# Optimization experiments

Hardware: AMD Instinct MI355X
Metric: run time of the kernel (lower is better)

Reference implementation:

```python
import jax, jax.numpy as jnp
import numpy as np

N0, N1, N2 = 409600, 40960, 4096   # source / mid / target node counts per sampled layer
E1, E2 = 409600, 40960             # edges in layer 1 / layer 2
F_IN, F_HID, F_OUT = 512, 256, 128


def setup_inputs() -> dict:
    key = jax.random.key(0)
    ks = jax.random.split(key, 12)
    s = 1.0 / np.sqrt(F_IN)
    s2 = 1.0 / np.sqrt(F_HID)
    return {
        "x": jax.random.normal(ks[0], (N0, F_IN), dtype=jnp.float32),
        "ei1_src": jax.random.randint(ks[1], (E1,), 0, N0),
        "ei1_dst": jax.random.randint(ks[2], (E1,), 0, N1),
        "ei2_src": jax.random.randint(ks[3], (E2,), 0, N1),
        "ei2_dst": jax.random.randint(ks[4], (E2,), 0, N2),
        "W1l": jax.random.uniform(ks[5], (F_IN, F_HID), jnp.float32, -s, s),
        "b1": jax.random.uniform(ks[6], (F_HID,), jnp.float32, -s, s),
        "W1r": jax.random.uniform(ks[7], (F_IN, F_HID), jnp.float32, -s, s),
        "W2l": jax.random.uniform(ks[8], (F_HID, F_OUT), jnp.float32, -s2, s2),
        "b2": jax.random.uniform(ks[9], (F_OUT,), jnp.float32, -s2, s2),
        "W2r": jax.random.uniform(ks[10], (F_HID, F_OUT), jnp.float32, -s2, s2),
    }


def _sage(x_src, src, dst, n_dst, Wl, b, Wr):
    # PyG SAGEConv (mean aggr): out = lin_l(mean_j x_j) + lin_r(x_target)
    msg = x_src[src]                                           # [E, F] gather
    agg = jax.ops.segment_sum(msg, dst, num_segments=n_dst)    # [n_dst, F]
    cnt = jax.ops.segment_sum(jnp.ones((src.shape[0],), x_src.dtype), dst,
                              num_segments=n_dst)
    mean = agg / jnp.maximum(cnt, 1.0)[:, None]
    x_dst = x_src[:n_dst]                                      # targets are first
    return mean @ Wl + b + x_dst @ Wr


def reference(x, ei1_src, ei1_dst, ei2_src, ei2_dst, W1l, b1, W1r, W2l, b2, W2r):
    h = _sage(x, ei1_src, ei1_dst, N1, W1l, b1, W1r)           # [N1, F_HID]
    h = jax.nn.relu(h)                                         # dropout = identity (eval)
    out = _sage(h, ei2_src, ei2_dst, N2, W2l, b2, W2r)         # [N2, F_OUT]
    return out
```

## Files before the change

kernel.cpp:

```cpp
#include <hip/hip_runtime.h>
#include <hip/hip_bf16.h>

#define N0 409600
#define N1 40960
#define N2 4096
#define E1c 409600
#define E2c 40960
#define F_IN 512
#define F_HID 256
#define F_OUT 128

using bf16x8 = __attribute__((ext_vector_type(8))) short;
using f32x4  = __attribute__((ext_vector_type(4))) float;

__device__ __forceinline__ ushort f2bf(float f) {
    union { float f; unsigned u; } v; v.f = f;
    unsigned r = v.u + 0x7fffu + ((v.u >> 16) & 1u);
    return (ushort)(r >> 16);
}
__device__ __forceinline__ float bf2f(ushort b) {
    union { unsigned u; float f; } v; v.u = ((unsigned)b) << 16;
    return v.f;
}

__device__ __forceinline__ bf16x8 load8(const ushort* p) {
    return *(const bf16x8*)p;
}
__device__ __forceinline__ bf16x8 load8(const float* p) {
    float4 a = *(const float4*)p;
    float4 b = *(const float4*)(p + 4);
    bf16x8 r;
    r[0] = (short)f2bf(a.x); r[1] = (short)f2bf(a.y);
    r[2] = (short)f2bf(a.z); r[3] = (short)f2bf(a.w);
    r[4] = (short)f2bf(b.x); r[5] = (short)f2bf(b.y);
    r[6] = (short)f2bf(b.z); r[7] = (short)f2bf(b.w);
    return r;
}

__global__ void k_prep(const int* __restrict__ dst1, int* __restrict__ cnt1,
                       const int* __restrict__ dst2, int* __restrict__ cnt2,
                       const float* __restrict__ W1l, const float* __restrict__ W1r,
                       const float* __restrict__ W2l, const float* __restrict__ W2r,
                       ushort* __restrict__ W1lT, ushort* __restrict__ W1rT,
                       ushort* __restrict__ W2lT, ushort* __restrict__ W2rT) {
    int idx = blockIdx.x * blockDim.x + threadIdx.x;
    if (idx < E1c) atomicAdd(&cnt1[dst1[idx]], 1);
    else if (idx - E1c < E2c) atomicAdd(&cnt2[dst2[idx - E1c]], 1);
    const int S1 = F_IN * F_HID;
    const int S2 = F_HID * F_OUT;
    if (idx < S1) {
        int k = idx / F_HID, n = idx % F_HID;
        W1lT[(size_t)n * F_IN + k] = f2bf(W1l[idx]);
    } else if (idx < 2 * S1) {
        int j = idx - S1;
        int k = j / F_HID, n = j % F_HID;
        W1rT[(size_t)n * F_IN + k] = f2bf(W1r[j]);
    } else if (idx < 2 * S1 + S2) {
        int j = idx - 2 * S1;
        int k = j / F_OUT, n = j % F_OUT;
        W2lT[(size_t)n * F_HID + k] = f2bf(W2l[j]);
    } else if (idx < 2 * S1 + 2 * S2) {
        int j = idx - 2 * S1 - S2;
        int k = j / F_OUT, n = j % F_OUT;
        W2rT[(size_t)n * F_HID + k] = f2bf(W2r[j]);
    }
}

#define NBLK1 (N1 / 1024)
#define NBLK2 (N2 / 1024)

__global__ __launch_bounds__(1024) void k_scanA2(const int* __restrict__ cnt1, int* __restrict__ off1,
                                                 int* __restrict__ bsum1,
                                                 const int* __restrict__ cnt2, int* __restrict__ off2,
                                                 int* __restrict__ bsum2) {
    __shared__ int wsum[16];
    int blk = blockIdx.x;
    const int* cnt; int* off; int* bsum; int lb;
    if (blk < NBLK1) { cnt = cnt1; off = off1; bsum = bsum1; lb = blk; }
    else             { cnt = cnt2; off = off2; bsum = bsum2; lb = blk - NBLK1; }
    int t = threadIdx.x, lane = t & 63, w = t >> 6;
    int i = lb * 1024 + t;
    int v = cnt[i];
    int s = v;
#pragma unroll
    for (int d = 1; d < 64; d <<= 1) {
        int u = __shfl_up(s, d, 64);
        if (lane >= d) s += u;
    }
    if (lane == 63) wsum[w] = s;
    __syncthreads();
    int wpre = 0, total = 0;
#pragma unroll
    for (int j = 0; j < 16; j++) {
        int u = wsum[j];
        if (j < w) wpre += u;
        total += u;
    }
    off[i] = wpre + (s - v);
    if (t == 0) bsum[lb] = total;
}

__global__ __launch_bounds__(1024) void k_scanB2(int* __restrict__ off1, int* __restrict__ cur1,
                                                 const int* __restrict__ bsum1,
                                                 int* __restrict__ off2, int* __restrict__ cur2,
                                                 const int* __restrict__ bsum2) {
    __shared__ int s_pre, s_tot;
    int blk = blockIdx.x;
    int* off; int* cur; const int* bsum; int lb, nblk, n;
    if (blk < NBLK1) { off = off1; cur = cur1; bsum = bsum1; lb = blk;         nblk = NBLK1; n = N1; }
    else             { off = off2; cur = cur2; bsum = bsum2; lb = blk - NBLK1; nblk = NBLK2; n = N2; }
    int t = threadIdx.x;
    if (t < 64) {
        int v = (t < nblk) ? bsum[t] : 0;
        int p = (t < lb) ? v : 0;
        int tt = v;
#pragma unroll
        for (int d = 32; d >= 1; d >>= 1) {
            p  += __shfl_xor(p, d, 64);
            tt += __shfl_xor(tt, d, 64);
        }
        if (t == 0) { s_pre = p; s_tot = tt; }
    }
    __syncthreads();
    int i = lb * 1024 + t;
    int val = off[i] + s_pre;
    off[i] = val;
    cur[i] = val;
    if (lb == 0 && t == 0) off[n] = s_tot;
}

__global__ void k_scatter2(const int* __restrict__ src1, const int* __restrict__ dst1,
                           int* __restrict__ cur1, int* __restrict__ perm1,
                           const int* __restrict__ src2, const int* __restrict__ dst2,
                           int* __restrict__ cur2, int* __restrict__ perm2) {
    int e = blockIdx.x * blockDim.x + threadIdx.x;
    if (e < E1c) {
        int d = dst1[e];
        int pos = atomicAdd(&cur1[d], 1);
        perm1[pos] = src1[e];
    } else {
        int e2 = e - E1c;
        if (e2 < E2c) {
            int d = dst2[e2];
            int pos = atomicAdd(&cur2[d], 1);
            perm2[pos] = src2[e2];
        }
    }
}

__global__ void k_agg1(const float* __restrict__ x, const int* __restrict__ perm,
                       const int* __restrict__ off, ushort* __restrict__ mean) {
    int d = blockIdx.x;
    int beg = off[d], end = off[d + 1];
    int t = threadIdx.x;
    const float4* xp = (const float4*)x;
    float ax = 0.f, ay = 0.f, az = 0.f, aw = 0.f;
    int e = beg;
    for (; e + 3 < end; e += 4) {
        int s0 = perm[e], s1 = perm[e + 1], s2 = perm[e + 2], s3 = perm[e + 3];
        float4 v0 = xp[(size_t)s0 * (F_IN / 4) + t];
        float4 v1 = xp[(size_t)s1 * (F_IN / 4) + t];
        float4 v2 = xp[(size_t)s2 * (F_IN / 4) + t];
        float4 v3 = xp[(size_t)s3 * (F_IN / 4) + t];
        ax += (v0.x + v1.x) + (v2.x + v3.x);
        ay += (v0.y + v1.y) + (v2.y + v3.y);
        az += (v0.z + v1.z) + (v2.z + v3.z);
        aw += (v0.w + v1.w) + (v2.w + v3.w);
    }
    for (; e < end; e++) {
        float4 v0 = xp[(size_t)perm[e] * (F_IN / 4) + t];
        ax += v0.x; ay += v0.y; az += v0.z; aw += v0.w;
    }
    int deg = end - beg;
    float inv = 1.0f / (float)(deg > 0 ? deg : 1);
    ushort4 o;
    o.x = f2bf(ax * inv); o.y = f2bf(ay * inv);
    o.z = f2bf(az * inv); o.w = f2bf(aw * inv);
    ((ushort4*)mean)[(size_t)d * (F_IN / 4) + t] = o;
}

__global__ void k_agg2(const ushort* __restrict__ h, const int* __restrict__ perm,
                       const int* __restrict__ off, ushort* __restrict__ mean) {
    int d = blockIdx.x;
    int beg = off[d], end = off[d + 1];
    int t = threadIdx.x;
    const ushort4* hp = (const ushort4*)h;
    float a0 = 0.f, a1 = 0.f, a2 = 0.f, a3 = 0.f;
    int e = beg;
    for (; e + 3 < end; e += 4) {
        ushort4 v = hp[(size_t)perm[e] * (F_HID / 4) + t];
        ushort4 u = hp[(size_t)perm[e + 1] * (F_HID / 4) + t];
        ushort4 w = hp[(size_t)perm[e + 2] * (F_HID / 4) + t];
        ushort4 z = hp[(size_t)perm[e + 3] * (F_HID / 4) + t];
        a0 += (bf2f(v.x) + bf2f(u.x)) + (bf2f(w.x) + bf2f(z.x));
        a1 += (bf2f(v.y) + bf2f(u.y)) + (bf2f(w.y) + bf2f(z.y));
        a2 += (bf2f(v.z) + bf2f(u.z)) + (bf2f(w.z) + bf2f(z.z));
        a3 += (bf2f(v.w) + bf2f(u.w)) + (bf2f(w.w) + bf2f(z.w));
    }
    for (; e < end; e++) {
        ushort4 v = hp[(size_t)perm[e] * (F_HID / 4) + t];
        a0 += bf2f(v.x); a1 += bf2f(v.y); a2 += bf2f(v.z); a3 += bf2f(v.w);
    }
    int deg = end - beg;
    float inv = 1.0f / (float)(deg > 0 ? deg : 1);
    ushort4 o;
    o.x = f2bf(a0 * inv); o.y = f2bf(a1 * inv);
    o.z = f2bf(a2 * inv); o.w = f2bf(a3 * inv);
    ((ushort4*)mean)[(size_t)d * (F_HID / 4) + t] = o;
}

#define GBK 32
#define APAD 8
template<int WM, int WN, int MF, int NF, typename TA2>
__global__ __launch_bounds__(256) void k_gemm(
    const ushort* __restrict__ A1, const TA2* __restrict__ A2,
    const ushort* __restrict__ B1T, const ushort* __restrict__ B2T,
    const float* __restrict__ bias, int M, int N, int K, int relu,
    ushort* __restrict__ Cb, float* __restrict__ Cf)
{
    constexpr int BM = WM * MF * 16;
    constexpr int BN = WN * NF * 16;
    static_assert(BM % 64 == 0 && BN % 64 == 0, "tile must be multiple of 64");
    __shared__ ushort As[BM][GBK + APAD];
    __shared__ ushort Bs[BN][GBK + APAD];
    int tid = threadIdx.x;
    int lane = tid & 63;
    int wid = tid >> 6;
    int wm = wid / WN, wn = wid % WN;
    int bm = blockIdx.x * BM, bn = blockIdx.y * BN;

    f32x4 acc[MF][NF];
#pragma unroll
    for (int i = 0; i < MF; i++)
#pragma unroll
        for (int j = 0; j < NF; j++) acc[i][j] = (f32x4){0.f, 0.f, 0.f, 0.f};

    int sr = tid >> 2;
    int sc = (tid & 3) * 8;

    for (int part = 0; part < 2; ++part) {
        const ushort* __restrict__ B = part ? B2T : B1T;
        for (int k0 = 0; k0 < K; k0 += GBK) {
#pragma unroll
            for (int i = 0; i < BM / 64; i++) {
                int r = sr + i * 64;
                bf16x8 av = part
                    ? load8(A2 + (size_t)(bm + r) * K + k0 + sc)
                    : load8(A1 + (size_t)(bm + r) * K + k0 + sc);
                *(bf16x8*)&As[r][sc] = av;
            }
#pragma unroll
            for (int i = 0; i < BN / 64; i++) {
                int r = sr + i * 64;
                *(bf16x8*)&Bs[r][sc] = load8(B + (size_t)(bn + r) * K + k0 + sc);
            }
            __syncthreads();
            bf16x8 af[MF], bfr[NF];
            int r0 = lane & 15;
            int kq = (lane >> 4) * 8;
#pragma unroll
            for (int i = 0; i < MF; i++)
                af[i] = *(const bf16x8*)&As[wm * (MF * 16) + i * 16 + r0][kq];
#pragma unroll
            for (int j = 0; j < NF; j++)
                bfr[j] = *(const bf16x8*)&Bs[wn * (NF * 16) + j * 16 + r0][kq];
#pragma unroll
            for (int i = 0; i < MF; i++)
#pragma unroll
                for (int j = 0; j < NF; j++)
                    acc[i][j] = __builtin_amdgcn_mfma_f32_16x16x32_bf16(af[i], bfr[j], acc[i][j], 0, 0, 0);
            __syncthreads();
        }
    }

    int cn0 = lane & 15;
    int rq = (lane >> 4) * 4;
#pragma unroll
    for (int i = 0; i < MF; i++) {
#pragma unroll
        for (int j = 0; j < NF; j++) {
            int col = bn + wn * (NF * 16) + j * 16 + cn0;
            float bv = bias[col];
#pragma unroll
            for (int rr = 0; rr < 4; rr++) {
                int row = bm + wm * (MF * 16) + i * 16 + rq + rr;
                float v = acc[i][j][rr] + bv;
                if (relu) v = fmaxf(v, 0.f);
                if (Cb) Cb[(size_t)row * N + col] = f2bf(v);
                if (Cf) Cf[(size_t)row * N + col] = v;
            }
        }
    }
}

static inline size_t align256(size_t x) { return (x + 255) & ~(size_t)255; }

extern "C" void kernel_launch(void* const* d_in, const int* in_sizes, int n_in,
                              void* d_out, int out_size, void* d_ws, size_t ws_size,
                              hipStream_t stream) {
    const float* x = (const float*)d_in[0];
    const int* ei1_src = (const int*)d_in[1];
    const int* ei1_dst = (const int*)d_in[2];
    const int* ei2_src = (const int*)d_in[3];
    const int* ei2_dst = (const int*)d_in[4];
    const float* W1l = (const float*)d_in[5];
    const float* b1 = (const float*)d_in[6];
    const float* W1r = (const float*)d_in[7];
    const float* W2l = (const float*)d_in[8];
    const float* b2 = (const float*)d_in[9];
    const float* W2r = (const float*)d_in[10];
    float* out = (float*)d_out;

    char* p = (char*)d_ws;
    size_t o = 0;
    int* cnt1 = (int*)(p + o); o += (size_t)N1 * 4;
    int* cnt2 = (int*)(p + o); o = align256(o + (size_t)N2 * 4);
    int* off1 = (int*)(p + o); o = align256(o + (size_t)(N1 + 1) * 4);
    int* cur1 = (int*)(p + o); o = align256(o + (size_t)N1 * 4);
    int* perm1 = (int*)(p + o); o = align256(o + (size_t)E1c * 4);
    int* off2 = (int*)(p + o); o = align256(o + (size_t)(N2 + 1) * 4);
    int* cur2 = (int*)(p + o); o = align256(o + (size_t)N2 * 4);
    int* perm2 = (int*)(p + o); o = align256(o + (size_t)E2c * 4);
    int* bsum1 = (int*)(p + o); o = align256(o + 64 * 4);
    int* bsum2 = (int*)(p + o); o = align256(o + 64 * 4);
    ushort* mean1 = (ushort*)(p + o); o = align256(o + (size_t)N1 * F_IN * 2);
    ushort* h     = (ushort*)(p + o); o = align256(o + (size_t)N1 * F_HID * 2);
    ushort* mean2 = (ushort*)(p + o); o = align256(o + (size_t)N2 * F_HID * 2);
    ushort* W1lT  = (ushort*)(p + o); o = align256(o + (size_t)F_IN * F_HID * 2);
    ushort* W1rT  = (ushort*)(p + o); o = align256(o + (size_t)F_IN * F_HID * 2);
    ushort* W2lT  = (ushort*)(p + o); o = align256(o + (size_t)F_HID * F_OUT * 2);
    ushort* W2rT  = (ushort*)(p + o); o = align256(o + (size_t)F_HID * F_OUT * 2);

    hipMemsetAsync(cnt1, 0, (size_t)(N1 + N2) * 4, stream);

    {
        int total = E1c + E2c;
        k_prep<<<(total + 255) / 256, 256, 0, stream>>>(
            ei1_dst, cnt1, ei2_dst, cnt2,
            W1l, W1r, W2l, W2r, W1lT, W1rT, W2lT, W2rT);
    }
    k_scanA2<<<NBLK1 + NBLK2, 1024, 0, stream>>>(cnt1, off1, bsum1, cnt2, off2, bsum2);
    k_scanB2<<<NBLK1 + NBLK2, 1024, 0, stream>>>(off1, cur1, bsum1, off2, cur2, bsum2);
    k_scatter2<<<(E1c + E2c + 255) / 256, 256, 0, stream>>>(
        ei1_src, ei1_dst, cur1, perm1, ei2_src, ei2_dst, cur2, perm2);

    k_agg1<<<N1, F_IN / 4, 0, stream>>>(x, perm1, off1, mean1);
    {
        dim3 grid(N1 / 64, F_HID / 256);
        k_gemm<1, 4, 4, 4, float><<<grid, 256, 0, stream>>>(mean1, x, W1lT, W1rT, b1,
                                                            N1, F_HID, F_IN, 1, h, nullptr);
    }

    k_agg2<<<N2, F_HID / 4, 0, stream>>>(h, perm2, off2, mean2);
    {
        dim3 grid(N2 / 64, F_OUT / 64);
        k_gemm<2, 2, 2, 2, ushort><<<grid, 256, 0, stream>>>(mean2, h, W2lT, W2rT, b2,
                                                             N2, F_OUT, F_HID, 0, nullptr, out);
    }
}
```

Measured before the change: 274.1 us.

## Fuse neighbor mean aggregation into SAGE GEMM kernel via shared-memory A tile

Replaces the separate aggregation kernels and GEMM kernels with one fused kernel per layer. Each block gathers and averages neighbor rows for 32 destination nodes straight into shared memory, then runs the MFMA GEMM against both weight matrices. This removes the write and re-read of the mean buffers and two launches. In exchange the tile is smaller (32 rows), so weight tiles are reloaded more often. The layer-2 grid is also small (128 blocks), and the gather and GEMM phases run serially within each block.

New measurement: 329.4 us. 1.2x slower.

```diff
diff --git a/kernel.cpp b/kernel.cpp
--- a/kernel.cpp
+++ b/kernel.cpp
@@ -23,18 +23,24 @@
     return v.f;
 }
 
-__device__ __forceinline__ bf16x8 load8(const ushort* p) {
-    return *(const bf16x8*)p;
-}
-__device__ __forceinline__ bf16x8 load8(const float* p) {
-    float4 a = *(const float4*)p;
-    float4 b = *(const float4*)(p + 4);
-    bf16x8 r;
-    r[0] = (short)f2bf(a.x); r[1] = (short)f2bf(a.y);
-    r[2] = (short)f2bf(a.z); r[3] = (short)f2bf(a.w);
-    r[4] = (short)f2bf(b.x); r[5] = (short)f2bf(b.y);
-    r[6] = (short)f2bf(b.z); r[7] = (short)f2bf(b.w);
-    return r;
+__device__ __forceinline__ void acc_row(const float* rowp, int lane, float* a) {
+    const float4* q = (const float4*)rowp + lane * 2;
+    float4 u = q[0], v = q[1];
+    a[0] += u.x; a[1] += u.y; a[2] += u.z; a[3] += u.w;
+    a[4] += v.x; a[5] += v.y; a[6] += v.z; a[7] += v.w;
+}
+__device__ __forceinline__ void acc_row(const ushort* rowp, int lane, float* a) {
+    ushort4 u = ((const ushort4*)rowp)[lane];
+    a[0] += bf2f(u.x); a[1] += bf2f(u.y); a[2] += bf2f(u.z); a[3] += bf2f(u.w);
+}
+__device__ __forceinline__ void stage_ax(const float* g, ushort* l) {
+    float4 v = *(const float4*)g;
+    ushort4 o;
+    o.x = f2bf(v.x); o.y = f2bf(v.y); o.z = f2bf(v.z); o.w = f2bf(v.w);
+    *(ushort4*)l = o;
+}
+__device__ __forceinline__ void stage_ax(const ushort* g, ushort* l) {
+    *(ushort4*)l = *(const ushort4*)g;
 }
 
 __global__ void k_prep(const int* __restrict__ dst1, int* __restrict__ cnt1,
@@ -148,119 +154,87 @@
     }
 }
 
-__global__ void k_agg1(const float* __restrict__ x, const int* __restrict__ perm,
-                       const int* __restrict__ off, ushort* __restrict__ mean) {
-    int d = blockIdx.x;
-    int beg = off[d], end = off[d + 1];
-    int t = threadIdx.x;
-    const float4* xp = (const float4*)x;
-    float ax = 0.f, ay = 0.f, az = 0.f, aw = 0.f;
-    int e = beg;
-    for (; e + 3 < end; e += 4) {
-        int s0 = perm[e], s1 = perm[e + 1], s2 = perm[e + 2], s3 = perm[e + 3];
-        float4 v0 = xp[(size_t)s0 * (F_IN / 4) + t];
-        float4 v1 = xp[(size_t)s1 * (F_IN / 4) + t];
-        float4 v2 = xp[(size_t)s2 * (F_IN / 4) + t];
-        float4 v3 = xp[(size_t)s3 * (F_IN / 4) + t];
-        ax += (v0.x + v1.x) + (v2.x + v3.x);
-        ay += (v0.y + v1.y) + (v2.y + v3.y);
-        az += (v0.z + v1.z) + (v2.z + v3.z);
-        aw += (v0.w + v1.w) + (v2.w + v3.w);
-    }
-    for (; e < end; e++) {
-        float4 v0 = xp[(size_t)perm[e] * (F_IN / 4) + t];
-        ax += v0.x; ay += v0.y; az += v0.z; aw += v0.w;
-    }
-    int deg = end - beg;
-    float inv = 1.0f / (float)(deg > 0 ? deg : 1);
-    ushort4 o;
-    o.x = f2bf(ax * inv); o.y = f2bf(ay * inv);
-    o.z = f2bf(az * inv); o.w = f2bf(aw * inv);
-    ((ushort4*)mean)[(size_t)d * (F_IN / 4) + t] = o;
-}
-
-__global__ void k_agg2(const ushort* __restrict__ h, const int* __restrict__ perm,
-                       const int* __restrict__ off, ushort* __restrict__ mean) {
-    int d = blockIdx.x;
-    int beg = off[d], end = off[d + 1];
-    int t = threadIdx.x;
-    const ushort4* hp = (const ushort4*)h;
-    float a0 = 0.f, a1 = 0.f, a2 = 0.f, a3 = 0.f;
-    int e = beg;
-    for (; e + 3 < end; e += 4) {
-        ushort4 v = hp[(size_t)perm[e] * (F_HID / 4) + t];
-        ushort4 u = hp[(size_t)perm[e + 1] * (F_HID / 4) + t];
-        ushort4 w = hp[(size_t)perm[e + 2] * (F_HID / 4) + t];
-        ushort4 z = hp[(size_t)perm[e + 3] * (F_HID / 4) + t];
-        a0 += (bf2f(v.x) + bf2f(u.x)) + (bf2f(w.x) + bf2f(z.x));
-        a1 += (bf2f(v.y) + bf2f(u.y)) + (bf2f(w.y) + bf2f(z.y));
-        a2 += (bf2f(v.z) + bf2f(u.z)) + (bf2f(w.z) + bf2f(z.z));
-        a3 += (bf2f(v.w) + bf2f(u.w)) + (bf2f(w.w) + bf2f(z.w));
-    }
-    for (; e < end; e++) {
-        ushort4 v = hp[(size_t)perm[e] * (F_HID / 4) + t];
-        a0 += bf2f(v.x); a1 += bf2f(v.y); a2 += bf2f(v.z); a3 += bf2f(v.w);
-    }
-    int deg = end - beg;
-    float inv = 1.0f / (float)(deg > 0 ? deg : 1);
-    ushort4 o;
-    o.x = f2bf(a0 * inv); o.y = f2bf(a1 * inv);
-    o.z = f2bf(a2 * inv); o.w = f2bf(a3 * inv);
-    ((ushort4*)mean)[(size_t)d * (F_HID / 4) + t] = o;
-}
-
-#define GBK 32
-#define APAD 8
-template<int WM, int WN, int MF, int NF, typename TA2>
-__global__ __launch_bounds__(256) void k_gemm(
-    const ushort* __restrict__ A1, const TA2* __restrict__ A2,
-    const ushort* __restrict__ B1T, const ushort* __restrict__ B2T,
-    const float* __restrict__ bias, int M, int N, int K, int relu,
-    ushort* __restrict__ Cb, float* __restrict__ Cf)
+template<int BN, int K, int WN, typename TSRC, bool RELU, bool OUTF32>
+__global__ __launch_bounds__(256) void k_sage(
+    const TSRC* __restrict__ src,
+    const int* __restrict__ perm, const int* __restrict__ off,
+    const ushort* __restrict__ BlT, const ushort* __restrict__ BrT,
+    const float* __restrict__ bias,
+    ushort* __restrict__ outb, float* __restrict__ outf)
 {
-    constexpr int BM = WM * MF * 16;
-    constexpr int BN = WN * NF * 16;
-    static_assert(BM % 64 == 0 && BN % 64 == 0, "tile must be multiple of 64");
-    __shared__ ushort As[BM][GBK + APAD];
-    __shared__ ushort Bs[BN][GBK + APAD];
+    constexpr int WM = 4 / WN;
+    constexpr int MF = 2 / WM;
+    constexpr int NF = BN / (WN * 16);
+    constexpr int FPL = (sizeof(TSRC) == 4) ? 8 : 4;
+
+    __shared__ ushort Am[32][K + 8];
+    __shared__ ushort Bs[BN][40];
+    __shared__ ushort Ax[32][40];
+
     int tid = threadIdx.x;
     int lane = tid & 63;
-    int wid = tid >> 6;
-    int wm = wid / WN, wn = wid % WN;
-    int bm = blockIdx.x * BM, bn = blockIdx.y * BN;
-
+    int w = tid >> 6;
+    int bm = blockIdx.x * 32;
+
+    for (int rr = 0; rr < 8; rr++) {
+        int row = w * 8 + rr;
+        int d = bm + row;
+        int beg = off[d], end = off[d + 1];
+        float a[FPL];
+#pragma unroll
+        for (int j = 0; j < FPL; j++) a[j] = 0.f;
+        int e = beg;
+        for (; e + 3 < end; e += 4) {
+            int s0 = perm[e], s1 = perm[e + 1], s2 = perm[e + 2], s3 = perm[e + 3];
+            acc_row(src + (size_t)s0 * K, lane, a);
+            acc_row(src + (size_t)s1 * K, lane, a);
+            acc_row(src + (size_t)s2 * K, lane, a);
+            acc_row(src + (size_t)s3 * K, lane, a);
+        }
+        for (; e < end; e++) acc_row(src + (size_t)perm[e] * K, lane, a);
+        int deg = end - beg;
+        float inv = 1.0f / (float)(deg > 0 ? deg : 1);
+        if constexpr (FPL == 8) {
+            bf16x8 o;
+#pragma unroll
+            for (int j = 0; j < 8; j++) o[j] = (short)f2bf(a[j] * inv);
+            *(bf16x8*)&Am[row][lane * 8] = o;
+        } else {
+            ushort4 o;
+            o.x = f2bf(a[0] * inv); o.y = f2bf(a[1] * inv);
+            o.z = f2bf(a[2] * inv); o.w = f2bf(a[3] * inv);
+            *(ushort4*)&Am[row][lane * 4] = o;
+        }
+    }
+    __syncthreads();
+
+    int wm = w / WN, wn = w % WN;
+    int sr = tid >> 2, sc = (tid & 3) * 8;
+    int r0 = lane & 15, kq = (lane >> 4) * 8;
     f32x4 acc[MF][NF];
 #pragma unroll
     for (int i = 0; i < MF; i++)
 #pragma unroll
         for (int j = 0; j < NF; j++) acc[i][j] = (f32x4){0.f, 0.f, 0.f, 0.f};
 
-    int sr = tid >> 2;
-    int sc = (tid & 3) * 8;
-
+#pragma unroll 1
     for (int part = 0; part < 2; ++part) {
-        const ushort* __restrict__ B = part ? B2T : B1T;
-        for (int k0 = 0; k0 < K; k0 += GBK) {
-#pragma unroll
-            for (int i = 0; i < BM / 64; i++) {
-                int r = sr + i * 64;
-                bf16x8 av = part
-                    ? load8(A2 + (size_t)(bm + r) * K + k0 + sc)
-                    : load8(A1 + (size_t)(bm + r) * K + k0 + sc);
-                *(bf16x8*)&As[r][sc] = av;
-            }
-#pragma unroll
-            for (int i = 0; i < BN / 64; i++) {
-                int r = sr + i * 64;
-                *(bf16x8*)&Bs[r][sc] = load8(B + (size_t)(bn + r) * K + k0 + sc);
+        const ushort* __restrict__ B = part ? BrT : BlT;
+        for (int k0 = 0; k0 < K; k0 += 32) {
+#pragma unroll
+            for (int i = 0; i < BN / 64; i++)
+                *(bf16x8*)&Bs[sr + i * 64][sc] =
+                    *(const bf16x8*)&B[(size_t)(sr + i * 64) * K + k0 + sc];
+            if (part) {
+                int r = tid >> 3, c = (tid & 7) * 4;
+                stage_ax(src + (size_t)(bm + r) * K + k0 + c, &Ax[r][c]);
             }
             __syncthreads();
             bf16x8 af[MF], bfr[NF];
-            int r0 = lane & 15;
-            int kq = (lane >> 4) * 8;
 #pragma unroll
             for (int i = 0; i < MF; i++)
-                af[i] = *(const bf16x8*)&As[wm * (MF * 16) + i * 16 + r0][kq];
+                af[i] = part ? *(const bf16x8*)&Ax[wm * (MF * 16) + i * 16 + r0][kq]
+                             : *(const bf16x8*)&Am[wm * (MF * 16) + i * 16 + r0][k0 + kq];
 #pragma unroll
             for (int j = 0; j < NF; j++)
                 bfr[j] = *(const bf16x8*)&Bs[wn * (NF * 16) + j * 16 + r0][kq];
@@ -279,15 +253,15 @@
     for (int i = 0; i < MF; i++) {
 #pragma unroll
         for (int j = 0; j < NF; j++) {
-            int col = bn + wn * (NF * 16) + j * 16 + cn0;
+            int col = wn * (NF * 16) + j * 16 + cn0;
             float bv = bias[col];
 #pragma unroll
             for (int rr = 0; rr < 4; rr++) {
                 int row = bm + wm * (MF * 16) + i * 16 + rq + rr;
                 float v = acc[i][j][rr] + bv;
-                if (relu) v = fmaxf(v, 0.f);
-                if (Cb) Cb[(size_t)row * N + col] = f2bf(v);
-                if (Cf) Cf[(size_t)row * N + col] = v;
+                if (RELU) v = fmaxf(v, 0.f);
+                if (OUTF32) outf[(size_t)row * BN + col] = v;
+                else        outb[(size_t)row * BN + col] = f2bf(v);
             }
         }
     }
@@ -323,13 +297,11 @@
     int* perm2 = (int*)(p + o); o = align256(o + (size_t)E2c * 4);
     int* bsum1 = (int*)(p + o); o = align256(o + 64 * 4);
     int* bsum2 = (int*)(p + o); o = align256(o + 64 * 4);
-    ushort* mean1 = (ushort*)(p + o); o = align256(o + (size_t)N1 * F_IN * 2);
-    ushort* h     = (ushort*)(p + o); o = align256(o + (size_t)N1 * F_HID * 2);
-    ushort* mean2 = (ushort*)(p + o); o = align256(o + (size_t)N2 * F_HID * 2);
-    ushort* W1lT  = (ushort*)(p + o); o = align256(o + (size_t)F_IN * F_HID * 2);
-    ushort* W1rT  = (ushort*)(p + o); o = align256(o + (size_t)F_IN * F_HID * 2);
-    ushort* W2lT  = (ushort*)(p + o); o = align256(o + (size_t)F_HID * F_OUT * 2);
-    ushort* W2rT  = (ushort*)(p + o); o = align256(o + (size_t)F_HID * F_OUT * 2);
+    ushort* h    = (ushort*)(p + o); o = align256(o + (size_t)N1 * F_HID * 2);
+    ushort* W1lT = (ushort*)(p + o); o = align256(o + (size_t)F_IN * F_HID * 2);
+    ushort* W1rT = (ushort*)(p + o); o = align256(o + (size_t)F_IN * F_HID * 2);
+    ushort* W2lT = (ushort*)(p + o); o = align256(o + (size_t)F_HID * F_OUT * 2);
+    ushort* W2rT = (ushort*)(p + o); o = align256(o + (size_t)F_HID * F_OUT * 2);
 
     hipMemsetAsync(cnt1, 0, (size_t)(N1 + N2) * 4, stream);
 
@@ -344,17 +316,9 @@
     k_scatter2<<<(E1c + E2c + 255) / 256, 256, 0, stream>>>(
         ei1_src, ei1_dst, cur1, perm1, ei2_src, ei2_dst, cur2, perm2);
 
-    k_agg1<<<N1, F_IN / 4, 0, stream>>>(x, perm1, off1, mean1);
-    {
-        dim3 grid(N1 / 64, F_HID / 256);
-        k_gemm<1, 4, 4, 4, float><<<grid, 256, 0, stream>>>(mean1, x, W1lT, W1rT, b1,
-                                                            N1, F_HID, F_IN, 1, h, nullptr);
-    }
-
-    k_agg2<<<N2, F_HID / 4, 0, stream>>>(h, perm2, off2, mean2);
-    {
-        dim3 grid(N2 / 64, F_OUT / 64);
-        k_gemm<2, 2, 2, 2, ushort><<<grid, 256, 0, stream>>>(mean2, h, W2lT, W2rT, b2,
-                                                             N2, F_OUT, F_HID, 0, nullptr, out);
-    }
-}
+    k_sage<256, 512, 4, float, true, false><<<N1 / 32, 256, 0, stream>>>(
+        x, perm1, off1, W1lT, W1rT, b1, h, nullptr);
+
+    k_sage<128, 256, 2, ushort, false, true><<<N2 / 32, 256, 0, stream>>>(
+        h, perm2, off2, W2lT, W2rT, b2, nullptr, out);
+}
```
